# Performance work log

Hardware: AMD Instinct MI355X
Metric: run time of the kernel (lower is better)

The kernel has to match this reference:

```python
import jax, jax.numpy as jnp
import numpy as np

N_NODES = 100000
N_EDGES = 3200000
IN_F = 500
HID = 64
OUT_F = 64
ALPHA = 0.1
K = 10


def setup_inputs() -> dict:
    key = jax.random.key(0)
    ks = jax.random.split(key, 8)
    x = jax.random.normal(ks[0], (N_NODES, IN_F), dtype=jnp.float32)
    edge_src = jax.random.randint(ks[1], (N_EDGES,), 0, N_NODES, dtype=jnp.int32)
    edge_dst = jax.random.randint(ks[2], (N_EDGES,), 0, N_NODES, dtype=jnp.int32)
    edge_weight = jax.random.uniform(ks[3], (N_EDGES,), dtype=jnp.float32)
    W1 = jax.random.normal(ks[4], (IN_F, HID), dtype=jnp.float32) * (1.0 / np.sqrt(IN_F))
    b1 = jnp.zeros((HID,), dtype=jnp.float32)
    W2 = jax.random.normal(ks[5], (HID, OUT_F), dtype=jnp.float32) * (1.0 / np.sqrt(HID))
    b2 = jnp.zeros((OUT_F,), dtype=jnp.float32)
    return {"x": x, "edge_src": edge_src, "edge_dst": edge_dst,
            "edge_weight": edge_weight, "W1": W1, "b1": b1, "W2": W2, "b2": b2}


def _spmm(edge_src, edge_dst, edge_weight, z):
    # sparse adj @ z : gather rows at src, scale by edge weight, scatter-add at dst
    msg = edge_weight[:, None] * z[edge_src]          # [E, C]
    return jax.ops.segment_sum(msg, edge_dst, num_segments=N_NODES)


def reference(x, edge_src, edge_dst, edge_weight, W1, b1, W2, b2):
    # MLP encoder (dropout is identity at inference)
    h = jax.nn.relu(x @ W1 + b1) @ W2 + b2            # [N, OUT_F]
    # APPNP propagation: z_{k+1} = (1-alpha) * A z_k + alpha * h
    z = h
    for _ in range(K):
        z = (1.0 - ALPHA) * _spmm(edge_src, edge_dst, edge_weight, z) + ALPHA * h
    return z
```

## Files before the change

### kernel.cpp

```cpp
#include <hip/hip_runtime.h>

#define N_NODES 100000
#define N_EDGES 3200000
#define IN_F 500
#define HID 64
#define OUT_F 64
#define ALPHA 0.1f
#define K_ITERS 10
#define SCAN_B ((N_NODES + 255) / 256)

typedef unsigned short ushort_t;
typedef unsigned int uint_t;

__device__ __forceinline__ float bf2f(ushort_t v) {
    union { uint_t u; float f; } c; c.u = ((uint_t)v) << 16; return c.f;
}
__device__ __forceinline__ ushort_t f2b(float f) {
    union { float f; uint_t u; } c; c.f = f;
    uint_t u = c.u + 0x7fffu + ((c.u >> 16) & 1u);
    return (ushort_t)(u >> 16);
}
__device__ __forceinline__ float bflo(uint_t u) {
    union { uint_t u; float f; } c; c.u = u << 16; return c.f;
}
__device__ __forceinline__ float bfhi(uint_t u) {
    union { uint_t u; float f; } c; c.u = u & 0xffff0000u; return c.f;
}
__device__ __forceinline__ uint_t packbf(float a, float b) {
    return (uint_t)f2b(a) | ((uint_t)f2b(b) << 16);
}

__global__ __launch_bounds__(256) void mlp_kernel(
    const float* __restrict__ x, const float* __restrict__ W1,
    const float* __restrict__ b1, const float* __restrict__ W2,
    const float* __restrict__ b2, ushort_t* __restrict__ hb,
    ushort_t* __restrict__ ahb)
{
    __shared__ float xs[32][100];
    __shared__ float hid[32][64];

    const int tid = threadIdx.x;
    const int c   = tid & 63;
    const int rg  = tid >> 6;
    const int block_row = blockIdx.x * 32;

    float acc[8] = {0.f, 0.f, 0.f, 0.f, 0.f, 0.f, 0.f, 0.f};

    for (int kb = 0; kb < IN_F; kb += 100) {
        for (int i = tid; i < 800; i += 256) {
            int r = i / 25, c4 = i - r * 25;
            *(float4*)&xs[r][c4 * 4] =
                *(const float4*)&x[(long)(block_row + r) * IN_F + kb + c4 * 4];
        }
        __syncthreads();
        for (int k = 0; k < 100; k += 4) {
            float w0 = W1[(kb+k+0)*HID + c];
            float w1 = W1[(kb+k+1)*HID + c];
            float w2 = W1[(kb+k+2)*HID + c];
            float w3 = W1[(kb+k+3)*HID + c];
            #pragma unroll
            for (int r = 0; r < 8; ++r) {
                float4 xv = *(const float4*)&xs[rg*8+r][k];
                acc[r] = fmaf(xv.x, w0, acc[r]);
                acc[r] = fmaf(xv.y, w1, acc[r]);
                acc[r] = fmaf(xv.z, w2, acc[r]);
                acc[r] = fmaf(xv.w, w3, acc[r]);
            }
        }
        __syncthreads();
    }

    float b = b1[c];
    #pragma unroll
    for (int r = 0; r < 8; ++r)
        hid[rg*8+r][c] = fmaxf(acc[r] + b, 0.f);
    __syncthreads();

    float o[8] = {0.f, 0.f, 0.f, 0.f, 0.f, 0.f, 0.f, 0.f};
    for (int k = 0; k < HID; k += 4) {
        float w0 = W2[(k+0)*OUT_F + c], w1 = W2[(k+1)*OUT_F + c];
        float w2 = W2[(k+2)*OUT_F + c], w3 = W2[(k+3)*OUT_F + c];
        #pragma unroll
        for (int r = 0; r < 8; ++r) {
            float4 hv = *(const float4*)&hid[rg*8+r][k];
            o[r] = fmaf(hv.x, w0, o[r]);
            o[r] = fmaf(hv.y, w1, o[r]);
            o[r] = fmaf(hv.z, w2, o[r]);
            o[r] = fmaf(hv.w, w3, o[r]);
        }
    }
    float bb = b2[c];
    int r0 = block_row + rg * 8;
    #pragma unroll
    for (int r = 0; r < 8; ++r) {
        float v = o[r] + bb;
        hb[(r0+r)*64 + c]  = f2b(v);
        ahb[(r0+r)*64 + c] = f2b(ALPHA * v);
    }
}

__global__ __launch_bounds__(256) void zero_cnt(int* __restrict__ cnt)
{
    int i = blockIdx.x * 256 + threadIdx.x;
    if (i < N_NODES) cnt[i] = 0;
}

__global__ __launch_bounds__(256) void count_keys(
    const int* __restrict__ key, int* __restrict__ cnt)
{
    int i = blockIdx.x * 256 + threadIdx.x;
    if (i < N_EDGES) atomicAdd(&cnt[key[i]], 1);
}

__global__ __launch_bounds__(256) void scan_block_sums(
    const int* __restrict__ cnt, int* __restrict__ bsum)
{
    int i = blockIdx.x * 256 + threadIdx.x;
    int v = (i < N_NODES) ? cnt[i] : 0;
    for (int off = 32; off; off >>= 1) v += __shfl_down(v, off);
    __shared__ int ws_[4];
    if ((threadIdx.x & 63) == 0) ws_[threadIdx.x >> 6] = v;
    __syncthreads();
    if (threadIdx.x == 0) bsum[blockIdx.x] = ws_[0] + ws_[1] + ws_[2] + ws_[3];
}

__global__ __launch_bounds__(512) void scan_partials(
    const int* __restrict__ bsum, int* __restrict__ boff)
{
    int t = threadIdx.x;
    int v = (t < SCAN_B) ? bsum[t] : 0;
    int lane = t & 63, w = t >> 6;
    int x = v;
    for (int off = 1; off < 64; off <<= 1) {
        int y = __shfl_up(x, off);
        if (lane >= off) x += y;
    }
    __shared__ int wsum[8];
    if (lane == 63) wsum[w] = x;
    __syncthreads();
    if (w == 0) {
        int s = (lane < 8) ? wsum[lane] : 0;
        for (int off = 1; off < 8; off <<= 1) {
            int y = __shfl_up(s, off);
            if (lane >= off) s += y;
        }
        if (lane < 8) wsum[lane] = s;
    }
    __syncthreads();
    int wpre = (w == 0) ? 0 : wsum[w - 1];
    if (t < SCAN_B) boff[t] = wpre + x - v;
}

__global__ __launch_bounds__(256) void scan_final(
    const int* __restrict__ cnt, const int* __restrict__ boff,
    int* __restrict__ row_start, int* __restrict__ pos)
{
    int i = blockIdx.x * 256 + threadIdx.x;
    int v = (i < N_NODES) ? cnt[i] : 0;
    int lane = threadIdx.x & 63, w = threadIdx.x >> 6;
    int x = v;
    for (int off = 1; off < 64; off <<= 1) {
        int y = __shfl_up(x, off);
        if (lane >= off) x += y;
    }
    __shared__ int wsum[4];
    if (lane == 63) wsum[w] = x;
    __syncthreads();
    int wpre = 0;
    for (int ww = 0; ww < w; ++ww) wpre += wsum[ww];
    int excl = wpre + x - v;
    int r = boff[blockIdx.x] + excl;
    if (i < N_NODES) { row_start[i] = r; pos[i] = r; }
    if (i == 0) row_start[N_NODES] = N_EDGES;
}

__global__ __launch_bounds__(256) void fill_dst(
    const int* __restrict__ esrc, const int* __restrict__ edst,
    const float* __restrict__ ew, int* __restrict__ pos,
    int2* __restrict__ csr)
{
    int i = blockIdx.x * 256 + threadIdx.x;
    if (i < N_EDGES) {
        int d = edst[i];
        int q = atomicAdd(&pos[d], 1);
        float w = 0.9f * ew[i];
        csr[q] = make_int2(esrc[i], __float_as_int(w));
    }
}

__global__ __launch_bounds__(256) void sort_rows(
    const int* __restrict__ row_start, int2* __restrict__ csr)
{
    const int node = blockIdx.x * 4 + (threadIdx.x >> 6);
    const int lane = threadIdx.x & 63;
    const int s0 = row_start[node];
    const int s1 = row_start[node + 1];
    int n = s1 - s0; if (n > 64) n = 64;
    int key = 0x7fffffff;
    int val = 0;
    if (lane < n) { int2 e = csr[s0 + lane]; key = e.x; val = e.y; }
    #pragma unroll
    for (int k = 2; k <= 64; k <<= 1) {
        #pragma unroll
        for (int j = k >> 1; j > 0; j >>= 1) {
            int pk = __shfl_xor(key, j, 64);
            int pv = __shfl_xor(val, j, 64);
            bool lower   = (lane & j) == 0;
            bool asc     = (lane & k) == 0;
            bool takeMin = (lower == asc);
            bool pick    = takeMin ? (pk < key) : (pk > key);
            if (pick) { key = pk; val = pv; }
        }
    }
    if (lane < n) csr[s0 + lane] = make_int2(key, val);
}

template <bool FINAL>
__global__ __launch_bounds__(256) void spmm_kernel(
    const int* __restrict__ row_start, const int2* __restrict__ csr,
    const ushort_t* __restrict__ zin, const ushort_t* __restrict__ ahb,
    void* __restrict__ zout)
{
    const int node = blockIdx.x * 4 + (threadIdx.x >> 6);
    const int lane = threadIdx.x & 63;
    const int g = lane >> 3;
    const int q = lane & 7;
    const int s0 = __builtin_amdgcn_readfirstlane(row_start[node]);
    const int s1 = __builtin_amdgcn_readfirstlane(row_start[node + 1]);

    float a0=0.f,a1=0.f,a2=0.f,a3=0.f,a4=0.f,a5=0.f,a6=0.f,a7=0.f;
    if (g == 0) {
        uint4 t = *(const uint4*)&ahb[node * 64 + 8 * q];
        a0 = bflo(t.x); a1 = bfhi(t.x); a2 = bflo(t.y); a3 = bfhi(t.y);
        a4 = bflo(t.z); a5 = bfhi(t.z); a6 = bflo(t.w); a7 = bfhi(t.w);
    }

#define FMA8(WV, ZV) do { \
        a0 = fmaf((WV), bflo((ZV).x), a0); a1 = fmaf((WV), bfhi((ZV).x), a1); \
        a2 = fmaf((WV), bflo((ZV).y), a2); a3 = fmaf((WV), bfhi((ZV).y), a3); \
        a4 = fmaf((WV), bflo((ZV).z), a4); a5 = fmaf((WV), bfhi((ZV).z), a5); \
        a6 = fmaf((WV), bflo((ZV).w), a6); a7 = fmaf((WV), bfhi((ZV).w), a7); \
    } while (0)

    int j = s0;
    for (; j + 32 <= s1; j += 32) {
        int2 e0 = csr[j + g];
        int2 e1 = csr[j + 8 + g];
        int2 e2 = csr[j + 16 + g];
        int2 e3 = csr[j + 24 + g];
        uint4 z0 = *(const uint4*)&zin[e0.x * 64 + 8 * q];
        uint4 z1 = *(const uint4*)&zin[e1.x * 64 + 8 * q];
        uint4 z2 = *(const uint4*)&zin[e2.x * 64 + 8 * q];
        uint4 z3 = *(const uint4*)&zin[e3.x * 64 + 8 * q];
        float w0 = __int_as_float(e0.y);
        float w1 = __int_as_float(e1.y);
        float w2 = __int_as_float(e2.y);
        float w3 = __int_as_float(e3.y);
        FMA8(w0, z0);
        FMA8(w1, z1);
        FMA8(w2, z2);
        FMA8(w3, z3);
    }
    for (; j < s1; j += 8) {
        int2 e = make_int2(0, 0);
        int jj = j + g;
        if (jj < s1) e = csr[jj];
        uint4 zt = *(const uint4*)&zin[e.x * 64 + 8 * q];
        float wt = __int_as_float(e.y);
        FMA8(wt, zt);
    }
#undef FMA8

    #pragma unroll
    for (int m = 8; m <= 32; m <<= 1) {
        a0 += __shfl_xor(a0, m, 64); a1 += __shfl_xor(a1, m, 64);
        a2 += __shfl_xor(a2, m, 64); a3 += __shfl_xor(a3, m, 64);
        a4 += __shfl_xor(a4, m, 64); a5 += __shfl_xor(a5, m, 64);
        a6 += __shfl_xor(a6, m, 64); a7 += __shfl_xor(a7, m, 64);
    }

    if (g == 0) {
        if (FINAL) {
            float* op = (float*)zout + node * 64 + 8 * q;
            *(float4*)op       = make_float4(a0, a1, a2, a3);
            *(float4*)(op + 4) = make_float4(a4, a5, a6, a7);
        } else {
            uint4 pk;
            pk.x = packbf(a0, a1); pk.y = packbf(a2, a3);
            pk.z = packbf(a4, a5); pk.w = packbf(a6, a7);
            *(uint4*)&((ushort_t*)zout)[node * 64 + 8 * q] = pk;
        }
    }
}

extern "C" void kernel_launch(void* const* d_in, const int* in_sizes, int n_in,
                              void* d_out, int out_size, void* d_ws, size_t ws_size,
                              hipStream_t stream)
{
    const float* x    = (const float*)d_in[0];
    const int*   esrc = (const int*)d_in[1];
    const int*   edst = (const int*)d_in[2];
    const float* ew   = (const float*)d_in[3];
    const float* W1   = (const float*)d_in[4];
    const float* b1   = (const float*)d_in[5];
    const float* W2   = (const float*)d_in[6];
    const float* b2   = (const float*)d_in[7];
    float* out = (float*)d_out;

    char* p = (char*)d_ws;
    ushort_t* ahb = (ushort_t*)p;  p += (size_t)N_NODES * 64 * 2;
    ushort_t* hb  = (ushort_t*)p;  p += (size_t)N_NODES * 64 * 2;
    ushort_t* zB  = (ushort_t*)p;  p += (size_t)N_NODES * 64 * 2;
    int2*  csr     = (int2*)p;     p += (size_t)N_EDGES * 8;
    int* cnt       = (int*)p;      p += (size_t)N_NODES * 4;
    int* pos       = (int*)p;      p += (size_t)N_NODES * 4;
    int* row_start = (int*)p;      p += (size_t)(N_NODES + 1) * 4;
    int* bsum      = (int*)p;      p += (size_t)SCAN_B * 4;
    int* boff      = (int*)p;      p += (size_t)SCAN_B * 4;

    const int EB = (N_EDGES + 255) / 256;

    hipLaunchKernelGGL(mlp_kernel, dim3(N_NODES / 32), dim3(256), 0, stream,
                       x, W1, b1, W2, b2, hb, ahb);

    hipLaunchKernelGGL(zero_cnt, dim3(SCAN_B), dim3(256), 0, stream, cnt);
    hipLaunchKernelGGL(count_keys, dim3(EB), dim3(256), 0, stream, edst, cnt);
    hipLaunchKernelGGL(scan_block_sums, dim3(SCAN_B), dim3(256), 0, stream, cnt, bsum);
    hipLaunchKernelGGL(scan_partials, dim3(1), dim3(512), 0, stream, bsum, boff);
    hipLaunchKernelGGL(scan_final, dim3(SCAN_B), dim3(256), 0, stream,
                       cnt, boff, row_start, pos);
    hipLaunchKernelGGL(fill_dst, dim3(EB), dim3(256), 0, stream,
                       esrc, edst, ew, pos, csr);
    hipLaunchKernelGGL(sort_rows, dim3(N_NODES / 4), dim3(256), 0, stream,
                       row_start, csr);

    const ushort_t* zi = hb;
    for (int it = 0; it < K_ITERS - 1; ++it) {
        ushort_t* zo = (it % 2 == 0) ? zB : hb;
        hipLaunchKernelGGL((spmm_kernel<false>), dim3(N_NODES / 4), dim3(256), 0, stream,
                           row_start, csr, zi, ahb, (void*)zo);
        zi = zo;
    }
    hipLaunchKernelGGL((spmm_kernel<true>), dim3(N_NODES / 4), dim3(256), 0, stream,
                       row_start, csr, zi, ahb, (void*)out);
}
```

Before: 1.438 ms.

## Partition CSR fill by destination range to localize scatter writes and atomics

```diff
diff --git a/kernel.cpp b/kernel.cpp
--- a/kernel.cpp
+++ b/kernel.cpp
@@ -9,8 +9,13 @@
 #define K_ITERS 10
 #define SCAN_B ((N_NODES + 255) / 256)
 
+#define NPART 8
+#define PART_N (N_NODES / NPART)
+#define FILL_GRID 2048
+
 typedef unsigned short ushort_t;
 typedef unsigned int uint_t;
+typedef int iv4 __attribute__((ext_vector_type(4)));
 
 __device__ __forceinline__ float bf2f(ushort_t v) {
     union { uint_t u; float f; } c; c.u = ((uint_t)v) << 16; return c.f;
@@ -174,17 +179,33 @@
     if (i == 0) row_start[N_NODES] = N_EDGES;
 }
 
-__global__ __launch_bounds__(256) void fill_dst(
+__global__ __launch_bounds__(256) void fill_dst_part(
     const int* __restrict__ esrc, const int* __restrict__ edst,
     const float* __restrict__ ew, int* __restrict__ pos,
     int2* __restrict__ csr)
 {
-    int i = blockIdx.x * 256 + threadIdx.x;
-    if (i < N_EDGES) {
-        int d = edst[i];
-        int q = atomicAdd(&pos[d], 1);
-        float w = 0.9f * ew[i];
-        csr[q] = make_int2(esrc[i], __float_as_int(w));
+    const int part = blockIdx.x & (NPART - 1);
+    const int lo = part * PART_N;
+    const int hi = lo + PART_N;
+    const int pthreads = (FILL_GRID / NPART) * 256;
+    const int NQUAD = N_EDGES / 4;
+
+    for (int qd = (blockIdx.x >> 3) * 256 + threadIdx.x; qd < NQUAD; qd += pthreads) {
+        iv4 d4 = __builtin_nontemporal_load((const iv4*)edst + qd);
+        const int i0 = qd * 4;
+#define DO_EDGE(DV, IDX) do {                                        \
+        int d_ = (DV);                                               \
+        if (d_ >= lo && d_ < hi) {                                   \
+            int   s_ = __builtin_nontemporal_load(&esrc[IDX]);       \
+            float w_ = __builtin_nontemporal_load(&ew[IDX]);         \
+            int   q_ = atomicAdd(&pos[d_], 1);                       \
+            csr[q_] = make_int2(s_, __float_as_int(0.9f * w_));      \
+        } } while (0)
+        DO_EDGE(d4.x, i0 + 0);
+        DO_EDGE(d4.y, i0 + 1);
+        DO_EDGE(d4.z, i0 + 2);
+        DO_EDGE(d4.w, i0 + 3);
+#undef DO_EDGE
     }
 }
 
@@ -329,7 +350,7 @@
     hipLaunchKernelGGL(scan_partials, dim3(1), dim3(512), 0, stream, bsum, boff);
     hipLaunchKernelGGL(scan_final, dim3(SCAN_B), dim3(256), 0, stream,
                        cnt, boff, row_start, pos);
-    hipLaunchKernelGGL(fill_dst, dim3(EB), dim3(256), 0, stream,
+    hipLaunchKernelGGL(fill_dst_part, dim3(FILL_GRID), dim3(256), 0, stream,
                        esrc, edst, ew, pos, csr);
     hipLaunchKernelGGL(sort_rows, dim3(N_NODES / 4), dim3(256), 0, stream,
                        row_start, csr);
```

Result: faster. 1.395 ms (-3.0%).
